# Kernel tuning notes

Measured on AMD Instinct MI355X. Metric: run time of the kernel, lower is better.

The kernel has to match this reference:

```python
import jax, jax.numpy as jnp
import numpy as np

NA, H, DIN, E, NN, ED = 1024, 128, 172, 256, 100000, 1
REG = 0.1
_gl_nodes = np.array([-0.1834346424956498, -0.525532409916329, -0.7966664774136267, -0.9602898564975363,
                      0.1834346424956498, 0.525532409916329, 0.7966664774136267, 0.9602898564975363], np.float32)
_gl_w = np.array([0.362683783378362, 0.3137066458778873, 0.2223810344533745, 0.1012285362903763] * 2, np.float32)
T_NODES = jnp.asarray(0.5 * (_gl_nodes + 1.0))    # tau = 1.0
T_WEIGHTS = jnp.asarray(0.5 * _gl_w)


def _rmsnorm(x, scale, eps=1e-8):
    rms = jnp.sqrt(jnp.sum(x * x, axis=-1, keepdims=True)) / np.sqrt(x.shape[-1])
    return scale * x / (rms + eps)


def setup_inputs() -> dict:
    key = jax.random.key(0)
    ks = jax.random.split(key, 16)
    s = 0.02
    return {
        "L_agg": 0.1 * jax.random.normal(ks[0], (NA, NA), jnp.float32),
        "delta_L_agg": 0.1 * jax.random.normal(ks[1], (NA, NA), jnp.float32),
        "x_sub": jax.random.normal(ks[2], (NA, DIN), jnp.float32),
        "m1_vec": jax.random.normal(ks[3], (NN, H), jnp.float32),
        "m2_vec": jax.random.normal(ks[4], (NN, H), jnp.float32),
        "names_table": jnp.zeros((NN, ED), jnp.float32),  # typ='Nil' static embedding
        "rms1_scale": jnp.ones((H,), jnp.float32),
        "rms2_scale": jnp.ones((H,), jnp.float32),
        "W_tune": s * jax.random.normal(ks[5], (DIN + 2 * ED, H), jnp.float32),
        "b_tune": jnp.zeros((H,), jnp.float32),
        "W_B1": s * jax.random.normal(ks[6], (H, H), jnp.float32),
        "b_B1": jnp.zeros((H,), jnp.float32),
        "W_B2": s * jax.random.normal(ks[7], (H, H), jnp.float32),
        "b_B2": jnp.zeros((H,), jnp.float32),
        "W_dt": 0.01 * jax.random.normal(ks[8], (H, 1), jnp.float32),
        "b_dt": -3.0 + 0.5 * jax.random.normal(ks[9], (1,), jnp.float32),  # softplus(b) small, like _init_dt_bias
        "A_log_1": jax.random.normal(ks[10], (H,), jnp.float32),
        "A_log_2": jax.random.normal(ks[11], (H,), jnp.float32),
        "target_src": jax.random.randint(ks[12], (E,), 0, NN),
        "target_dst": jax.random.randint(ks[13], (E,), 0, NN),
        "active_input_ids": jax.random.randint(ks[14], (NA,), 0, NN),
    }


def reference(L_agg, delta_L_agg, x_sub, m1_vec, m2_vec, names_table,
              rms1_scale, rms2_scale, W_tune, b_tune, W_B1, b_B1, W_B2, b_B2,
              W_dt, b_dt, A_log_1, A_log_2, target_src, target_dst, active_input_ids):
    n = L_agg.shape[0]
    I = jnp.eye(n, dtype=L_agg.dtype)
    # ZOH discretization of the graph Laplacian operator
    As_bar = I - REG * delta_L_agg + REG ** 2 * (delta_L_agg @ (L_agg + delta_L_agg / 2))
    dt = delta_L_agg[None] * T_NODES[:, None, None]                       # [8,n,n]
    LHS = I[None] - REG * dt + REG ** 2 * (dt @ (L_agg[None] + dt / 2))   # [8,n,n]
    P_L_inv = I - REG * L_agg
    # static-embedding neighbor info (zeros for 'Nil', done faithfully)
    neigh = jnp.zeros((n, 2 * ED), L_agg.dtype)
    neigh = neigh.at[:E, :ED].set(names_table[target_src])
    neigh = neigh.at[:E, ED:].set(names_table[target_dst])
    neigh = neigh.at[E:2 * E, :ED].set(names_table[target_dst])
    neigh = neigh.at[E:2 * E, ED:].set(names_table[target_src])
    x_in = jnp.concatenate([x_sub, neigh], axis=1)
    zt = x_in @ W_tune + b_tune                                           # TuneInput
    ztn = _rmsnorm(zt, rms1_scale)
    Bzt = ztn @ W_B1 + b_B1
    delta_1 = jax.nn.softplus(ztn @ W_dt + b_dt)                          # [n,1] broadcasts over H
    dA1 = delta_1 * (-jnp.exp(A_log_1))                                   # [n,H]
    At_bar_1 = jnp.exp(dA1)
    C_1 = (P_L_inv @ (Bzt * delta_1))[None] * T_WEIGHTS[:, None, None]    # [8,n,H]
    RHS_1 = jnp.exp(dA1[None] * T_NODES[:, None, None])                   # [8,n,H]
    integral_1 = jnp.sum((LHS @ C_1) * RHS_1, axis=0)                     # GL quadrature
    m1 = m1_vec[active_input_ids]
    updated_c_1 = As_bar @ (m1 * At_bar_1) + integral_1
    # second selective-SSM stage (reconstructed symmetrically from truncation)
    u_2 = zt + jax.nn.gelu(updated_c_1, approximate=True)
    u_2n = _rmsnorm(u_2, rms2_scale)
    But = u_2n @ W_B2 + b_B2
    delta_2 = jax.nn.softplus(u_2n @ W_dt + b_dt)
    dA2 = delta_2 * (-jnp.exp(A_log_2))
    At_bar_2 = jnp.exp(dA2)
    C_2 = (P_L_inv @ (But * delta_2))[None] * T_WEIGHTS[:, None, None]
    RHS_2 = jnp.exp(dA2[None] * T_NODES[:, None, None])
    integral_2 = jnp.sum((LHS @ C_2) * RHS_2, axis=0)
    m2 = m2_vec[active_input_ids]
    updated_c_2 = As_bar @ (m2 * At_bar_2) + integral_2
    return jnp.stack([updated_c_1, updated_c_2])                           # [2,n,H]
```

## Files before the change

kernel.cpp:

```cpp
#include <hip/hip_runtime.h>
#include <math.h>

#define N_A   1024
#define HDIM  128
#define DIN   172
#define E_CNT 256
#define LP    72

typedef __attribute__((ext_vector_type(8))) short bf16x8;
typedef __attribute__((ext_vector_type(4))) float f32x4;

__device__ __forceinline__ unsigned short f2bf(float x) {
    unsigned int u = __float_as_uint(x);
    unsigned int r = (u + 0x7fffu + ((u >> 16) & 1u)) >> 16;
    return (unsigned short)r;
}
__device__ __forceinline__ float bf2f(unsigned short x) {
    return __uint_as_float((unsigned int)x << 16);
}

__constant__ float c_t[8] = {
    0.4082826787521751f, 0.2372337950418355f, 0.10166676129318665f, 0.019855071751231843f,
    0.5917173212478249f, 0.7627662049581645f, 0.8983332387068134f, 0.9801449282487682f};
__constant__ float c_w[8] = {
    0.181341891689181f, 0.15685332293894365f, 0.11119051722668725f, 0.05061426814518815f,
    0.181341891689181f, 0.15685332293894365f, 0.11119051722668725f, 0.05061426814518815f};

__global__ __launch_bounds__(256)
void conv_all(const float* __restrict__ L, const float* __restrict__ dL,
              const float* __restrict__ x_sub, const float* __restrict__ names,
              const int* __restrict__ src, const int* __restrict__ dst,
              const float* __restrict__ W_tune, const float* __restrict__ W_B1,
              const float* __restrict__ W_B2,
              unsigned short* __restrict__ Lb, unsigned short* __restrict__ dLb,
              unsigned short* __restrict__ LbT, unsigned short* __restrict__ dLbT,
              unsigned short* __restrict__ Xb, unsigned short* __restrict__ WtT,
              unsigned short* __restrict__ WB1T, unsigned short* __restrict__ WB2T)
{
    __shared__ unsigned short tl[64][72];
    const int b = blockIdx.x, tid = threadIdx.x;
    if (b < 2048) {
        const int t = b * 256 + tid;
        const float* s = (t < 262144) ? L : dL;
        unsigned short* d = (t < 262144) ? Lb : dLb;
        const int q = (t < 262144) ? t : t - 262144;
        float4 v = *(const float4*)(s + (size_t)q * 4);
        ushort4 o;
        o.x = f2bf(v.x); o.y = f2bf(v.y); o.z = f2bf(v.z); o.w = f2bf(v.w);
        *(ushort4*)(d + (size_t)q * 4) = o;
    } else if (b < 2816) {
        const int t = (b - 2048) * 256 + tid;
        const int i = t / 192, k = t - i * 192;
        float val = 0.f;
        if (k < DIN) val = x_sub[(size_t)i * DIN + k];
        else if (k == DIN) {
            if (i < E_CNT)          val = names[src[i]];
            else if (i < 2 * E_CNT) val = names[dst[i - E_CNT]];
        } else if (k == DIN + 1) {
            if (i < E_CNT)          val = names[dst[i]];
            else if (i < 2 * E_CNT) val = names[src[i - E_CNT]];
        }
        Xb[t] = f2bf(val);
    } else if (b < 2912) {
        const int t = (b - 2816) * 256 + tid;
        const int j = t / 192, k = t - j * 192;
        WtT[t] = (k < DIN + 2) ? f2bf(W_tune[k * HDIM + j]) : (unsigned short)0;
    } else if (b < 3040) {
        const int t = (b - 2912) * 256 + tid;
        const int half = t >> 14, tt = t & 16383;
        const int j = tt >> 7, k = tt & 127;
        (half ? WB2T : WB1T)[tt] = f2bf((half ? W_B2 : W_B1)[k * HDIM + j]);
    } else {
        const int t = b - 3040;
        const float* s = (t < 256) ? L : dL;
        unsigned short* d = (t < 256) ? LbT : dLbT;
        const int tile = t & 255, tr = tile >> 4, tc = tile & 15;
        const int row = tid >> 2, cg = (tid & 3) << 4;
        #pragma unroll
        for (int e = 0; e < 4; ++e) {
            float4 v = *(const float4*)(s + (size_t)(tr * 64 + row) * 1024 + tc * 64 + cg + e * 4);
            tl[row][cg + e * 4 + 0] = f2bf(v.x);
            tl[row][cg + e * 4 + 1] = f2bf(v.y);
            tl[row][cg + e * 4 + 2] = f2bf(v.z);
            tl[row][cg + e * 4 + 3] = f2bf(v.w);
        }
        __syncthreads();
        unsigned short* drow = d + (size_t)(tc * 64 + row) * 1024 + tr * 64 + cg;
        #pragma unroll
        for (int e = 0; e < 4; ++e) {
            ushort4 o;
            o.x = tl[cg + e * 4 + 0][row];
            o.y = tl[cg + e * 4 + 1][row];
            o.z = tl[cg + e * 4 + 2][row];
            o.w = tl[cg + e * 4 + 3][row];
            *(ushort4*)(drow + e * 4) = o;
        }
    }
}

__device__ __forceinline__ void core_sa(
    const unsigned short* __restrict__ ag, const unsigned short* __restrict__ bg,
    unsigned short* As, unsigned short* Bs, int klen,
    int srow, int skc, int wrow, int wcol, int fr, int fk, f32x4 (&acc)[2][2])
{
    bf16x8 pa0 = *(const bf16x8*)ag, pa1 = *(const bf16x8*)(ag + 8);
    bf16x8 pb0 = *(const bf16x8*)bg, pb1 = *(const bf16x8*)(bg + 8);
    for (int k0 = 0; k0 < klen; k0 += 64) {
        __syncthreads();
        *(bf16x8*)&As[srow * LP + skc] = pa0; *(bf16x8*)&As[srow * LP + skc + 8] = pa1;
        *(bf16x8*)&Bs[srow * LP + skc] = pb0; *(bf16x8*)&Bs[srow * LP + skc + 8] = pb1;
        __syncthreads();
        if (k0 + 64 < klen) {
            pa0 = *(const bf16x8*)(ag + k0 + 64); pa1 = *(const bf16x8*)(ag + k0 + 72);
            pb0 = *(const bf16x8*)(bg + k0 + 64); pb1 = *(const bf16x8*)(bg + k0 + 72);
        }
        #pragma unroll
        for (int h = 0; h < 2; ++h) {
            const int ko = h * 32 + fk;
            bf16x8 a0 = *(const bf16x8*)&As[(wrow + fr) * LP + ko];
            bf16x8 a1 = *(const bf16x8*)&As[(wrow + 16 + fr) * LP + ko];
            bf16x8 b0 = *(const bf16x8*)&Bs[(wcol + fr) * LP + ko];
            bf16x8 b1 = *(const bf16x8*)&Bs[(wcol + 16 + fr) * LP + ko];
            acc[0][0] = __builtin_amdgcn_mfma_f32_16x16x32_bf16(a0, b0, acc[0][0], 0, 0, 0);
            acc[0][1] = __builtin_amdgcn_mfma_f32_16x16x32_bf16(a0, b1, acc[0][1], 0, 0, 0);
            acc[1][0] = __builtin_amdgcn_mfma_f32_16x16x32_bf16(a1, b0, acc[1][0], 0, 0, 0);
            acc[1][1] = __builtin_amdgcn_mfma_f32_16x16x32_bf16(a1, b1, acc[1][1], 0, 0, 0);
        }
    }
}

__global__ __launch_bounds__(256)
void k_d2(const unsigned short* __restrict__ LbT, const unsigned short* __restrict__ dLbT,
          const unsigned short* __restrict__ dLb,
          unsigned short* __restrict__ P1b, unsigned short* __restrict__ P2b,
          const unsigned short* __restrict__ Xb, const unsigned short* __restrict__ WtT,
          const float* __restrict__ b_tune, float* __restrict__ zt)
{
    __shared__ unsigned short shm[128 * LP];
    unsigned short* As = shm; unsigned short* Bs = shm + 64 * LP;
    const int bid = blockIdx.x, tid = threadIdx.x;
    const int srow = tid >> 2, skc = (tid & 3) << 4;
    const int lane = tid & 63, w = tid >> 6;
    const int wrow = (w >> 1) * 32, wcol = (w & 1) * 32;
    const int fr = lane & 15, fg = lane >> 4, fk = fg << 3;

    if (bid < 512) {
        const int bx = bid >> 4, rb = bid & 15;
        const int unit = bx >> 4, cb = bx & 15;
        const unsigned short* A = unit ? dLbT : LbT;
        unsigned short* O = unit ? P2b : P1b;
        const unsigned short* ag = A   + (size_t)(rb * 64 + srow) * 1024 + skc;
        const unsigned short* bg = dLb + (size_t)(cb * 64 + srow) * 1024 + skc;
        f32x4 acc[2][2] = {};
        core_sa(ag, bg, As, Bs, 1024, srow, skc, wrow, wcol, fr, fk, acc);
        #pragma unroll
        for (int m = 0; m < 2; ++m) {
            const int gm = rb * 64 + wrow + m * 16 + fg * 4;
            #pragma unroll
            for (int n = 0; n < 2; ++n) {
                const int gj = cb * 64 + wcol + n * 16 + fr;
                ushort4 tv;
                tv.x = f2bf(acc[m][n][0]); tv.y = f2bf(acc[m][n][1]);
                tv.z = f2bf(acc[m][n][2]); tv.w = f2bf(acc[m][n][3]);
                *(ushort4*)&O[(size_t)gj * 1024 + gm] = tv;
            }
        }
    } else {
        const int t = bid - 512;
        const int cb = t >> 4, rb = t & 15;
        const unsigned short* ag = Xb  + (size_t)(rb * 64 + srow) * 192 + skc;
        const unsigned short* bg = WtT + (size_t)(cb * 64 + srow) * 192 + skc;
        f32x4 acc[2][2] = {};
        core_sa(ag, bg, As, Bs, 192, srow, skc, wrow, wcol, fr, fk, acc);
        #pragma unroll
        for (int m = 0; m < 2; ++m) {
            const int gm = rb * 64 + wrow + m * 16 + fg * 4;
            #pragma unroll
            for (int n = 0; n < 2; ++n) {
                const int gj = cb * 64 + wcol + n * 16 + fr;
                const float bb = b_tune[gj];
                #pragma unroll
                for (int r = 0; r < 4; ++r)
                    zt[(size_t)(gm + r) * HDIM + gj] = acc[m][n][r] + bb;
            }
        }
    }
}

__device__ __forceinline__ float rowsum128(float v, float* red, int j)
{
    #pragma unroll
    for (int o = 32; o > 0; o >>= 1) v += __shfl_xor(v, o, 64);
    if ((j & 63) == 0) red[j >> 6] = v;
    __syncthreads();
    const float t = red[0] + red[1];
    __syncthreads();
    return t;
}

__device__ __forceinline__ void rms_core(
    float x, int i, int j,
    const float* rms_scale, const float* W_dt, const float* b_dt,
    const float* A_log, const float* m_vec, const int* act,
    unsigned short* xnb, float* VU, unsigned short* VUt, float* dlt, float* red)
{
    const float ss = rowsum128(x * x, red, j);
    const float rms = sqrtf(ss) * 0.08838834764831845f;
    const float xn = rms_scale[j] * x / (rms + 1e-8f);
    const float dsum = rowsum128(xn * W_dt[j], red, j);
    const float dd = dsum + b_dt[0];
    const float delta = dd > 0.f ? dd + log1pf(expf(-dd)) : log1pf(expf(dd));
    xnb[(size_t)i * HDIM + j] = f2bf(xn);
    const float U = m_vec[(size_t)act[i] * HDIM + j] * expf(-delta * expf(A_log[j]));
    VU[(size_t)i * 256 + 128 + j] = U;
    VUt[(size_t)(128 + j) * 1024 + i] = f2bf(U);
    if (j == 0) dlt[i] = delta;
}

__device__ __forceinline__ float post_elem(float y1, float y2, float y3, float s,
                                           float g, float u, float dA)
{
    const float bl = -0.1f * y1 + 0.01f * y2;
    const float cq = 0.005f * y3;
    float integ = 0.f;
    #pragma unroll
    for (int k = 0; k < 8; ++k) {
        const float t = c_t[k];
        integ += c_w[k] * (g + t * bl + t * t * cq) * expf(dA * t);
    }
    return u - 0.1f * s + integ;
}

__global__ __launch_bounds__(256)
void k_d3(const unsigned short* __restrict__ LbT,
          const unsigned short* __restrict__ P1b, const unsigned short* __restrict__ P2b,
          unsigned short* __restrict__ M2b, unsigned short* __restrict__ M3b,
          const float* __restrict__ zt,
          const float* __restrict__ rms1, const float* __restrict__ W_dt,
          const float* __restrict__ b_dt, const float* __restrict__ A1,
          const float* __restrict__ m1, const int* __restrict__ act,
          unsigned short* __restrict__ xnb, float* __restrict__ VU,
          unsigned short* __restrict__ VUt, float* __restrict__ dlt1)
{
    __shared__ unsigned short shm[128 * LP];
    const int bid = blockIdx.x, tid = threadIdx.x;

    if (bid < 512) {
        unsigned short* As = shm; unsigned short* Bs = shm + 64 * LP;
        const int srow = tid >> 2, skc = (tid & 3) << 4;
        const int lane = tid & 63, w = tid >> 6;
        const int wrow = (w >> 1) * 32, wcol = (w & 1) * 32;
        const int fr = lane & 15, fg = lane >> 4, fk = fg << 3;
        const int bx = bid >> 4, rb = bid & 15;
        const int unit = bx >> 4, cb = bx & 15;
        const unsigned short* Bt = unit ? P2b : P1b;
        const unsigned short* Src = unit ? P2b : P1b;
        unsigned short* O = unit ? M3b : M2b;
        const unsigned short* ag = LbT + (size_t)(rb * 64 + srow) * 1024 + skc;
        const unsigned short* bg = Bt  + (size_t)(cb * 64 + srow) * 1024 + skc;
        f32x4 acc[2][2] = {};
        core_sa(ag, bg, As, Bs, 1024, srow, skc, wrow, wcol, fr, fk, acc);
        #pragma unroll
        for (int m = 0; m < 2; ++m) {
            const int gm = rb * 64 + wrow + m * 16 + fg * 4;
            #pragma unroll
            for (int n = 0; n < 2; ++n) {
                const int gj = cb * 64 + wcol + n * 16 + fr;
                ushort4 sv = *(const ushort4*)&Src[(size_t)gj * 1024 + gm];
                ushort4 tv;
                tv.x = f2bf(bf2f(sv.x) - 0.1f * acc[m][n][0]);
                tv.y = f2bf(bf2f(sv.y) - 0.1f * acc[m][n][1]);
                tv.z = f2bf(bf2f(sv.z) - 0.1f * acc[m][n][2]);
                tv.w = f2bf(bf2f(sv.w) - 0.1f * acc[m][n][3]);
                *(ushort4*)&O[(size_t)gj * 1024 + gm] = tv;
            }
        }
    } else {
        float* redf = (float*)shm;
        const int g = tid >> 7, j = tid & 127;
        const int i = (bid - 512) * 2 + g;
        rms_core(zt[(size_t)i * HDIM + j], i, j, rms1, W_dt, b_dt, A1, m1, act,
                 xnb, VU, VUt, dlt1, redf + 2 * g);
    }
}

__global__ __launch_bounds__(256)
void gemm_bz2(const unsigned short* __restrict__ xnb, const unsigned short* __restrict__ WBT,
              const float* __restrict__ b_B, const float* __restrict__ dlt,
              float* __restrict__ VU, unsigned short* __restrict__ VUt)
{
    const int cb = blockIdx.x, rb = blockIdx.y;
    __shared__ unsigned short As[64 * LP];
    __shared__ unsigned short Bs[64 * LP];
    const int tid = threadIdx.x, srow = tid >> 2, skc = (tid & 3) << 4;
    const unsigned short* ag = xnb + (size_t)(rb * 64 + srow) * HDIM + skc;
    const unsigned short* bg = WBT + (size_t)(cb * 64 + srow) * HDIM + skc;
    const int lane = tid & 63, w = tid >> 6;
    const int wrow = (w >> 1) * 32, wcol = (w & 1) * 32;
    const int fr = lane & 15, fg = lane >> 4, fk = fg << 3;

    f32x4 acc[2][2] = {};
    core_sa(ag, bg, As, Bs, 128, srow, skc, wrow, wcol, fr, fk, acc);

    #pragma unroll
    for (int m = 0; m < 2; ++m) {
        const int gm = rb * 64 + wrow + m * 16 + fg * 4;
        #pragma unroll
        for (int n = 0; n < 2; ++n) {
            const int col = cb * 64 + wcol + n * 16 + fr;
            const float bb = b_B[col];
            float vv[4];
            #pragma unroll
            for (int r = 0; r < 4; ++r) {
                vv[r] = (acc[m][n][r] + bb) * dlt[gm + r];
                VU[(size_t)(gm + r) * 256 + col] = vv[r];
            }
            ushort4 tv;
            tv.x = f2bf(vv[0]); tv.y = f2bf(vv[1]); tv.z = f2bf(vv[2]); tv.w = f2bf(vv[3]);
            *(ushort4*)&VUt[(size_t)col * 1024 + gm] = tv;
        }
    }
}

__global__ __launch_bounds__(256)
void k_big(const unsigned short* __restrict__ Lb, const unsigned short* __restrict__ dLb,
           const unsigned short* __restrict__ P1b, const unsigned short* __restrict__ P2b,
           const unsigned short* __restrict__ M2b, const unsigned short* __restrict__ M3b,
           const unsigned short* __restrict__ VUt, const float* __restrict__ VU,
           float* __restrict__ Gf, float* __restrict__ dLVf, float* __restrict__ P1Vf,
           float* __restrict__ Y2f, float* __restrict__ Y3f, float* __restrict__ dLUf,
           float* __restrict__ P1Uf, float* __restrict__ P2Uf)
{
    __shared__ unsigned short shm[96 * LP];
    unsigned short* AsL = shm;
    unsigned short* Bs  = shm + 32 * LP;

    const int bid = blockIdx.x, tid = threadIdx.x;
    const int unit = bid >> 6, rem = bid & 63;
    const int rb = rem >> 1, cb = rem & 1;

    const unsigned short* A;
    float* O;
    switch (unit) {
        case 0: A = Lb;  O = Gf;   break;
        case 1: A = dLb; O = dLVf; break;
        case 2: A = P1b; O = P1Vf; break;
        case 3: A = M2b; O = Y2f;  break;
        case 4: A = M3b; O = Y3f;  break;
        case 5: A = dLb; O = dLUf; break;
        case 6: A = P1b; O = P1Uf; break;
        default: A = P2b; O = P2Uf; break;
    }
    const int bn0 = ((unit >= 5) ? 128 : 0) + cb * 64;

    const int sar = tid >> 3, sac = (tid & 7) << 3;
    const int sbr = tid >> 2, sbc = (tid & 3) << 4;

    const unsigned short* ag = A   + (size_t)(rb * 32 + sar) * 1024 + sac;
    const unsigned short* bg = VUt + (size_t)(bn0 + sbr) * 1024 + sbc;

    const int lane = tid & 63, w = tid >> 6;
    const int fr = lane & 15, fg = lane >> 4, fk = fg << 3;

    f32x4 acc[2] = {};
    bf16x8 pa = *(const bf16x8*)ag;
    bf16x8 pb0 = *(const bf16x8*)bg, pb1 = *(const bf16x8*)(bg + 8);

    for (int k0 = 0; k0 < 1024; k0 += 64) {
        __syncthreads();
        *(bf16x8*)&AsL[sar * LP + sac] = pa;
        *(bf16x8*)&Bs[sbr * LP + sbc] = pb0; *(bf16x8*)&Bs[sbr * LP + sbc + 8] = pb1;
        __syncthreads();
        if (k0 + 64 < 1024) {
            pa = *(const bf16x8*)(ag + k0 + 64);
            pb0 = *(const bf16x8*)(bg + k0 + 64); pb1 = *(const bf16x8*)(bg + k0 + 72);
        }
        #pragma unroll
        for (int h = 0; h < 2; ++h) {
            const int ko = h * 32 + fk;
            bf16x8 a0 = *(const bf16x8*)&AsL[fr * LP + ko];
            bf16x8 a1 = *(const bf16x8*)&AsL[(16 + fr) * LP + ko];
            bf16x8 b0 = *(const bf16x8*)&Bs[(w * 16 + fr) * LP + ko];
            acc[0] = __builtin_amdgcn_mfma_f32_16x16x32_bf16(a0, b0, acc[0], 0, 0, 0);
            acc[1] = __builtin_amdgcn_mfma_f32_16x16x32_bf16(a1, b0, acc[1], 0, 0, 0);
        }
    }

    #pragma unroll
    for (int m = 0; m < 2; ++m) {
        const int gm = rb * 32 + m * 16 + fg * 4;
        const int gj = cb * 64 + w * 16 + fr;
        if (unit == 0) {
            #pragma unroll
            for (int r = 0; r < 4; ++r)
                O[(size_t)(gm + r) * 128 + gj] =
                    VU[(size_t)(gm + r) * 256 + gj] - 0.1f * acc[m][r];
        } else {
            #pragma unroll
            for (int r = 0; r < 4; ++r)
                O[(size_t)(gm + r) * 128 + gj] = acc[m][r];
        }
    }
}

__global__ __launch_bounds__(256)
void k_mid(const float* __restrict__ Gf, const float* __restrict__ dLVf,
           const float* __restrict__ P1Vf, const float* __restrict__ Y2f,
           const float* __restrict__ Y3f, const float* __restrict__ dLUf,
           const float* __restrict__ P1Uf, const float* __restrict__ P2Uf,
           const float* __restrict__ zt, const float* __restrict__ dlt1,
           const float* __restrict__ A1,
           const float* __restrict__ rms2, const float* __restrict__ W_dt,
           const float* __restrict__ b_dt, const float* __restrict__ A2,
           const float* __restrict__ m2, const int* __restrict__ act,
           unsigned short* __restrict__ xnb, float* __restrict__ VU,
           unsigned short* __restrict__ VUt, float* __restrict__ dlt2,
           float* __restrict__ out0)
{
    __shared__ float redf[4];
    const int tid = threadIdx.x;
    const int g = tid >> 7, j = tid & 127;
    const int i = blockIdx.x * 2 + g;
    const int idx = i * HDIM + j;

    const float y1 = dLVf[idx] - 0.1f * P1Vf[idx];
    const float s  = dLUf[idx] - 0.1f * P1Uf[idx] - 0.05f * P2Uf[idx];
    const float dA = -dlt1[i] * expf(A1[j]);
    const float o1 = post_elem(y1, Y2f[idx], Y3f[idx], s, Gf[idx],
                               VU[(size_t)i * 256 + 128 + j], dA);
    out0[idx] = o1;
    const float g3 = o1 * o1 * o1;
    const float gel = 0.5f * o1 * (1.0f + tanhf(0.7978845608028654f * (o1 + 0.044715f * g3)));
    const float x = zt[idx] + gel;

    rms_core(x, i, j, rms2, W_dt, b_dt, A2, m2, act, xnb, VU, VUt, dlt2, redf + 2 * g);
}

__global__ __launch_bounds__(256)
void k_tail(const float* __restrict__ Gf, const float* __restrict__ dLVf,
            const float* __restrict__ P1Vf, const float* __restrict__ Y2f,
            const float* __restrict__ Y3f, const float* __restrict__ dLUf,
            const float* __restrict__ P1Uf, const float* __restrict__ P2Uf,
            const float* __restrict__ VU, const float* __restrict__ dlt,
            const float* __restrict__ A_log, float* __restrict__ out)
{
    const int idx = blockIdx.x * 256 + threadIdx.x;
    const int i = idx >> 7, j = idx & 127;
    const float y1 = dLVf[idx] - 0.1f * P1Vf[idx];
    const float s  = dLUf[idx] - 0.1f * P1Uf[idx] - 0.05f * P2Uf[idx];
    const float dA = -dlt[i] * expf(A_log[j]);
    out[idx] = post_elem(y1, Y2f[idx], Y3f[idx], s, Gf[idx],
                         VU[(size_t)i * 256 + 128 + j], dA);
}

extern "C" void kernel_launch(void* const* d_in, const int* in_sizes, int n_in,
                              void* d_out, int out_size, void* d_ws, size_t ws_size,
                              hipStream_t stream)
{
    const float* L      = (const float*)d_in[0];
    const float* dL     = (const float*)d_in[1];
    const float* x_sub  = (const float*)d_in[2];
    const float* m1     = (const float*)d_in[3];
    const float* m2     = (const float*)d_in[4];
    const float* names  = (const float*)d_in[5];
    const float* rms1   = (const float*)d_in[6];
    const float* rms2   = (const float*)d_in[7];
    const float* W_tune = (const float*)d_in[8];
    const float* b_tune = (const float*)d_in[9];
    const float* W_B1   = (const float*)d_in[10];
    const float* b_B1   = (const float*)d_in[11];
    const float* W_B2   = (const float*)d_in[12];
    const float* b_B2   = (const float*)d_in[13];
    const float* W_dt   = (const float*)d_in[14];
    const float* b_dt   = (const float*)d_in[15];
    const float* A1     = (const float*)d_in[16];
    const float* A2     = (const float*)d_in[17];
    const int*   src    = (const int*)d_in[18];
    const int*   dst    = (const int*)d_in[19];
    const int*   act    = (const int*)d_in[20];
    float* out = (float*)d_out;

    float* ws    = (float*)d_ws;
    float* zt    = ws;
    float* VU    = zt    + 131072;
    float* Gf    = VU    + 262144;
    float* dLVf  = Gf    + 131072;
    float* P1Vf  = dLVf  + 131072;
    float* Y2f   = P1Vf  + 131072;
    float* Y3f   = Y2f   + 131072;
    float* dLUf  = Y3f   + 131072;
    float* P1Uf  = dLUf  + 131072;
    float* P2Uf  = P1Uf  + 131072;
    float* dlt1  = P2Uf  + 131072;
    float* dlt2  = dlt1  + 1024;
    unsigned short* Lb    = (unsigned short*)(dlt2 + 1024);
    unsigned short* dLb   = Lb    + 1048576;
    unsigned short* LbT   = dLb   + 1048576;
    unsigned short* dLbT  = LbT   + 1048576;
    unsigned short* M2b   = dLbT;
    unsigned short* P1b   = dLbT  + 1048576;
    unsigned short* P2b   = P1b   + 1048576;
    unsigned short* M3b   = P2b   + 1048576;
    unsigned short* VUt   = M3b   + 1048576;
    unsigned short* Xb    = VUt   + 262144;
    unsigned short* WtT   = Xb    + 196608;
    unsigned short* WB1T  = WtT   + 24576;
    unsigned short* WB2T  = WB1T  + 16384;
    unsigned short* xnb   = WB2T  + 16384;

    conv_all<<<dim3(3552), dim3(256), 0, stream>>>(
        L, dL, x_sub, names, src, dst, W_tune, W_B1, W_B2,
        Lb, dLb, LbT, dLbT, Xb, WtT, WB1T, WB2T);

    k_d2<<<dim3(544), dim3(256), 0, stream>>>(
        LbT, dLbT, dLb, P1b, P2b, Xb, WtT, b_tune, zt);

    k_d3<<<dim3(1024), dim3(256), 0, stream>>>(
        LbT, P1b, P2b, M2b, M3b, zt,
        rms1, W_dt, b_dt, A1, m1, act, xnb, VU, VUt, dlt1);

    gemm_bz2<<<dim3(2, 16), dim3(256), 0, stream>>>(xnb, WB1T, b_B1, dlt1, VU, VUt);

    k_big<<<dim3(512), dim3(256), 0, stream>>>(
        Lb, dLb, P1b, P2b, M2b, M3b, VUt, VU,
        Gf, dLVf, P1Vf, Y2f, Y3f, dLUf, P1Uf, P2Uf);

    k_mid<<<dim3(512), dim3(256), 0, stream>>>(
        Gf, dLVf, P1Vf, Y2f, Y3f, dLUf, P1Uf, P2Uf,
        zt, dlt1, A1, rms2, W_dt, b_dt, A2, m2, act,
        xnb, VU, VUt, dlt2, out);

    gemm_bz2<<<dim3(2, 16), dim3(256), 0, stream>>>(xnb, WB2T, b_B2, dlt2, VU, VUt);

    k_big<<<dim3(512), dim3(256), 0, stream>>>(
        Lb, dLb, P1b, P2b, M2b, M3b, VUt, VU,
        Gf, dLVf, P1Vf, Y2f, Y3f, dLUf, P1Uf, P2Uf);

    k_tail<<<dim3(512), dim3(256), 0, stream>>>(
        Gf, dLVf, P1Vf, Y2f, Y3f, dLUf, P1Uf, P2Uf,
        VU, dlt2, A2, out + 131072);
}
```

Baseline: 77.46 us.

## Fuse RMSNorm/delta stage with B-projection GEMM, removing separate gemm_bz2 launches

Folds the RMSNorm, softplus delta and U computation together with the small xn@W_B GEMM into one task per 16-row by 64-column tile. Each block keeps the normalized rows in LDS and runs MFMA on them directly, so the xnb round trip and two kernel launches go away. The cost is that the row-wise norm is recomputed once for each of the two column blocks. The second-stage U moves to a separate U2 buffer so the fused kernel does not overwrite VU values still being read by other blocks.

```diff
diff --git a/kernel.cpp b/kernel.cpp
--- a/kernel.cpp
+++ b/kernel.cpp
@@ -198,25 +198,6 @@
     return t;
 }
 
-__device__ __forceinline__ void rms_core(
-    float x, int i, int j,
-    const float* rms_scale, const float* W_dt, const float* b_dt,
-    const float* A_log, const float* m_vec, const int* act,
-    unsigned short* xnb, float* VU, unsigned short* VUt, float* dlt, float* red)
-{
-    const float ss = rowsum128(x * x, red, j);
-    const float rms = sqrtf(ss) * 0.08838834764831845f;
-    const float xn = rms_scale[j] * x / (rms + 1e-8f);
-    const float dsum = rowsum128(xn * W_dt[j], red, j);
-    const float dd = dsum + b_dt[0];
-    const float delta = dd > 0.f ? dd + log1pf(expf(-dd)) : log1pf(expf(dd));
-    xnb[(size_t)i * HDIM + j] = f2bf(xn);
-    const float U = m_vec[(size_t)act[i] * HDIM + j] * expf(-delta * expf(A_log[j]));
-    VU[(size_t)i * 256 + 128 + j] = U;
-    VUt[(size_t)(128 + j) * 1024 + i] = f2bf(U);
-    if (j == 0) dlt[i] = delta;
-}
-
 __device__ __forceinline__ float post_elem(float y1, float y2, float y3, float s,
                                            float g, float u, float dA)
 {
@@ -229,6 +210,80 @@
         integ += c_w[k] * (g + t * bl + t * t * cq) * expf(dA * t);
     }
     return u - 0.1f * s + integ;
+}
+
+__device__ void rmsbz_task(int cb, int rb, int tid,
+    unsigned short* xnL , float* dltL , float* red ,
+    const float* zt,
+    const float* Gf, const float* dLVf, const float* P1Vf, const float* Y2f,
+    const float* Y3f, const float* dLUf, const float* P1Uf, const float* P2Uf,
+    const float* dlt_prev, const float* A_prev, float* out0,
+    const float* rms_scale, const float* W_dt, const float* b_dt,
+    const float* A_log, const float* m_vec, const int* act,
+    const unsigned short* WBT, const float* b_B,
+    float* VU, unsigned short* VUt, float* Udst, int ustride,
+    float* dlt_out)
+{
+    const int g = tid >> 7, j = tid & 127;
+
+    for (int rr = 0; rr < 8; ++rr) {
+        const int lr = g * 8 + rr;
+        const int row = rb * 16 + lr;
+        const int idx = row * HDIM + j;
+        float x;
+        if (!out0) {
+            x = zt[idx];
+        } else {
+            const float y1 = dLVf[idx] - 0.1f * P1Vf[idx];
+            const float s  = dLUf[idx] - 0.1f * P1Uf[idx] - 0.05f * P2Uf[idx];
+            const float dA = -dlt_prev[row] * expf(A_prev[j]);
+            const float o1 = post_elem(y1, Y2f[idx], Y3f[idx], s, Gf[idx],
+                                       VU[(size_t)row * 256 + 128 + j], dA);
+            if (cb == 0) out0[idx] = o1;
+            const float g3 = o1 * o1 * o1;
+            const float gel = 0.5f * o1 * (1.0f + tanhf(0.7978845608028654f * (o1 + 0.044715f * g3)));
+            x = zt[idx] + gel;
+        }
+        const float ss = rowsum128(x * x, red + 2 * g, j);
+        const float rms = sqrtf(ss) * 0.08838834764831845f;
+        const float xn = rms_scale[j] * x / (rms + 1e-8f);
+        const float ds = rowsum128(xn * W_dt[j], red + 2 * g, j);
+        const float dd = ds + b_dt[0];
+        const float delta = dd > 0.f ? dd + log1pf(expf(-dd)) : log1pf(expf(dd));
+        xnL[lr * 136 + j] = f2bf(xn);
+        if (j == 0) dltL[lr] = delta;
+        if (cb == 0) {
+            const float U = m_vec[(size_t)act[row] * HDIM + j] * expf(-delta * expf(A_log[j]));
+            Udst[(size_t)row * ustride + j] = U;
+            VUt[(size_t)(128 + j) * 1024 + row] = f2bf(U);
+            if (j == 0) dlt_out[row] = delta;
+        }
+    }
+    __syncthreads();
+
+    const int lane = tid & 63, w = tid >> 6;
+    const int fr = lane & 15, fg = lane >> 4, fk = fg << 3;
+    const int col = cb * 64 + w * 16 + fr;
+
+    f32x4 acc = {};
+    #pragma unroll
+    for (int ks = 0; ks < 4; ++ks) {
+        const int ko = ks * 32 + fk;
+        bf16x8 a = *(const bf16x8*)&xnL[fr * 136 + ko];
+        bf16x8 b = *(const bf16x8*)(WBT + (size_t)col * HDIM + ko);
+        acc = __builtin_amdgcn_mfma_f32_16x16x32_bf16(a, b, acc, 0, 0, 0);
+    }
+    const float bb = b_B[col];
+    const int r0 = fg * 4;
+    float vv[4];
+    #pragma unroll
+    for (int r = 0; r < 4; ++r) {
+        vv[r] = (acc[r] + bb) * dltL[r0 + r];
+        VU[(size_t)(rb * 16 + r0 + r) * 256 + col] = vv[r];
+    }
+    ushort4 tv;
+    tv.x = f2bf(vv[0]); tv.y = f2bf(vv[1]); tv.z = f2bf(vv[2]); tv.w = f2bf(vv[3]);
+    *(ushort4*)&VUt[(size_t)col * 1024 + rb * 16 + r0] = tv;
 }
 
 __global__ __launch_bounds__(256)
@@ -239,8 +294,9 @@
           const float* __restrict__ rms1, const float* __restrict__ W_dt,
           const float* __restrict__ b_dt, const float* __restrict__ A1,
           const float* __restrict__ m1, const int* __restrict__ act,
-          unsigned short* __restrict__ xnb, float* __restrict__ VU,
-          unsigned short* __restrict__ VUt, float* __restrict__ dlt1)
+          const unsigned short* __restrict__ WB1T, const float* __restrict__ b_B1,
+          float* __restrict__ VU, unsigned short* __restrict__ VUt,
+          float* __restrict__ dlt1)
 {
     __shared__ unsigned short shm[128 * LP];
     const int bid = blockIdx.x, tid = threadIdx.x;
@@ -254,7 +310,6 @@
         const int bx = bid >> 4, rb = bid & 15;
         const int unit = bx >> 4, cb = bx & 15;
         const unsigned short* Bt = unit ? P2b : P1b;
-        const unsigned short* Src = unit ? P2b : P1b;
         unsigned short* O = unit ? M3b : M2b;
         const unsigned short* ag = LbT + (size_t)(rb * 64 + srow) * 1024 + skc;
         const unsigned short* bg = Bt  + (size_t)(cb * 64 + srow) * 1024 + skc;
@@ -266,7 +321,7 @@
             #pragma unroll
             for (int n = 0; n < 2; ++n) {
                 const int gj = cb * 64 + wcol + n * 16 + fr;
-                ushort4 sv = *(const ushort4*)&Src[(size_t)gj * 1024 + gm];
+                ushort4 sv = *(const ushort4*)&Bt[(size_t)gj * 1024 + gm];
                 ushort4 tv;
                 tv.x = f2bf(bf2f(sv.x) - 0.1f * acc[m][n][0]);
                 tv.y = f2bf(bf2f(sv.y) - 0.1f * acc[m][n][1]);
@@ -276,49 +331,16 @@
             }
         }
     } else {
-        float* redf = (float*)shm;
-        const int g = tid >> 7, j = tid & 127;
-        const int i = (bid - 512) * 2 + g;
-        rms_core(zt[(size_t)i * HDIM + j], i, j, rms1, W_dt, b_dt, A1, m1, act,
-                 xnb, VU, VUt, dlt1, redf + 2 * g);
-    }
-}
-
-__global__ __launch_bounds__(256)
-void gemm_bz2(const unsigned short* __restrict__ xnb, const unsigned short* __restrict__ WBT,
-              const float* __restrict__ b_B, const float* __restrict__ dlt,
-              float* __restrict__ VU, unsigned short* __restrict__ VUt)
-{
-    const int cb = blockIdx.x, rb = blockIdx.y;
-    __shared__ unsigned short As[64 * LP];
-    __shared__ unsigned short Bs[64 * LP];
-    const int tid = threadIdx.x, srow = tid >> 2, skc = (tid & 3) << 4;
-    const unsigned short* ag = xnb + (size_t)(rb * 64 + srow) * HDIM + skc;
-    const unsigned short* bg = WBT + (size_t)(cb * 64 + srow) * HDIM + skc;
-    const int lane = tid & 63, w = tid >> 6;
-    const int wrow = (w >> 1) * 32, wcol = (w & 1) * 32;
-    const int fr = lane & 15, fg = lane >> 4, fk = fg << 3;
-
-    f32x4 acc[2][2] = {};
-    core_sa(ag, bg, As, Bs, 128, srow, skc, wrow, wcol, fr, fk, acc);
-
-    #pragma unroll
-    for (int m = 0; m < 2; ++m) {
-        const int gm = rb * 64 + wrow + m * 16 + fg * 4;
-        #pragma unroll
-        for (int n = 0; n < 2; ++n) {
-            const int col = cb * 64 + wcol + n * 16 + fr;
-            const float bb = b_B[col];
-            float vv[4];
-            #pragma unroll
-            for (int r = 0; r < 4; ++r) {
-                vv[r] = (acc[m][n][r] + bb) * dlt[gm + r];
-                VU[(size_t)(gm + r) * 256 + col] = vv[r];
-            }
-            ushort4 tv;
-            tv.x = f2bf(vv[0]); tv.y = f2bf(vv[1]); tv.z = f2bf(vv[2]); tv.w = f2bf(vv[3]);
-            *(ushort4*)&VUt[(size_t)col * 1024 + gm] = tv;
-        }
+        unsigned short* xnL = shm;
+        float* dltL = (float*)(shm + 16 * 136);
+        float* red  = dltL + 16;
+        const int t = bid - 512;
+        const int cb = t >> 6, rb = t & 63;
+        rmsbz_task(cb, rb, tid, xnL, dltL, red, zt,
+                   nullptr, nullptr, nullptr, nullptr, nullptr, nullptr, nullptr, nullptr,
+                   nullptr, nullptr, nullptr,
+                   rms1, W_dt, b_dt, A1, m1, act, WB1T, b_B1,
+                   VU, VUt, VU + 128, 256, dlt1);
     }
 }
 
@@ -413,27 +435,21 @@
            const float* __restrict__ rms2, const float* __restrict__ W_dt,
            const float* __restrict__ b_dt, const float* __restrict__ A2,
            const float* __restrict__ m2, const int* __restrict__ act,
-           unsigned short* __restrict__ xnb, float* __restrict__ VU,
-           unsigned short* __restrict__ VUt, float* __restrict__ dlt2,
+           const unsigned short* __restrict__ WB2T, const float* __restrict__ b_B2,
+           float* __restrict__ VU, unsigned short* __restrict__ VUt,
+           float* __restrict__ U2, float* __restrict__ dlt2,
            float* __restrict__ out0)
 {
-    __shared__ float redf[4];
-    const int tid = threadIdx.x;
-    const int g = tid >> 7, j = tid & 127;
-    const int i = blockIdx.x * 2 + g;
-    const int idx = i * HDIM + j;
-
-    const float y1 = dLVf[idx] - 0.1f * P1Vf[idx];
-    const float s  = dLUf[idx] - 0.1f * P1Uf[idx] - 0.05f * P2Uf[idx];
-    const float dA = -dlt1[i] * expf(A1[j]);
-    const float o1 = post_elem(y1, Y2f[idx], Y3f[idx], s, Gf[idx],
-                               VU[(size_t)i * 256 + 128 + j], dA);
-    out0[idx] = o1;
-    const float g3 = o1 * o1 * o1;
-    const float gel = 0.5f * o1 * (1.0f + tanhf(0.7978845608028654f * (o1 + 0.044715f * g3)));
-    const float x = zt[idx] + gel;
-
-    rms_core(x, i, j, rms2, W_dt, b_dt, A2, m2, act, xnb, VU, VUt, dlt2, redf + 2 * g);
+    __shared__ unsigned short shm[16 * 136 + 48];
+    unsigned short* xnL = shm;
+    float* dltL = (float*)(shm + 16 * 136);
+    float* red  = dltL + 16;
+    const int cb = blockIdx.x >> 6, rb = blockIdx.x & 63;
+    rmsbz_task(cb, rb, threadIdx.x, xnL, dltL, red, zt,
+               Gf, dLVf, P1Vf, Y2f, Y3f, dLUf, P1Uf, P2Uf,
+               dlt1, A1, out0,
+               rms2, W_dt, b_dt, A2, m2, act, WB2T, b_B2,
+               VU, VUt, U2, 128, dlt2);
 }
 
 __global__ __launch_bounds__(256)
@@ -441,7 +457,7 @@
             const float* __restrict__ P1Vf, const float* __restrict__ Y2f,
             const float* __restrict__ Y3f, const float* __restrict__ dLUf,
             const float* __restrict__ P1Uf, const float* __restrict__ P2Uf,
-            const float* __restrict__ VU, const float* __restrict__ dlt,
+            const float* __restrict__ U2, const float* __restrict__ dlt,
             const float* __restrict__ A_log, float* __restrict__ out)
 {
     const int idx = blockIdx.x * 256 + threadIdx.x;
@@ -449,8 +465,7 @@
     const float y1 = dLVf[idx] - 0.1f * P1Vf[idx];
     const float s  = dLUf[idx] - 0.1f * P1Uf[idx] - 0.05f * P2Uf[idx];
     const float dA = -dlt[i] * expf(A_log[j]);
-    out[idx] = post_elem(y1, Y2f[idx], Y3f[idx], s, Gf[idx],
-                         VU[(size_t)i * 256 + 128 + j], dA);
+    out[idx] = post_elem(y1, Y2f[idx], Y3f[idx], s, Gf[idx], U2[idx], dA);
 }
 
 extern "C" void kernel_launch(void* const* d_in, const int* in_sizes, int n_in,
@@ -483,7 +498,8 @@
     float* ws    = (float*)d_ws;
     float* zt    = ws;
     float* VU    = zt    + 131072;
-    float* Gf    = VU    + 262144;
+    float* U2    = VU    + 262144;
+    float* Gf    = U2    + 131072;
     float* dLVf  = Gf    + 131072;
     float* P1Vf  = dLVf  + 131072;
     float* Y2f   = P1Vf  + 131072;
@@ -506,7 +522,6 @@
     unsigned short* WtT   = Xb    + 196608;
     unsigned short* WB1T  = WtT   + 24576;
     unsigned short* WB2T  = WB1T  + 16384;
-    unsigned short* xnb   = WB2T  + 16384;
 
     conv_all<<<dim3(3552), dim3(256), 0, stream>>>(
         L, dL, x_sub, names, src, dst, W_tune, W_B1, W_B2,
@@ -515,22 +530,19 @@
     k_d2<<<dim3(544), dim3(256), 0, stream>>>(
         LbT, dLbT, dLb, P1b, P2b, Xb, WtT, b_tune, zt);
 
-    k_d3<<<dim3(1024), dim3(256), 0, stream>>>(
+    k_d3<<<dim3(640), dim3(256), 0, stream>>>(
         LbT, P1b, P2b, M2b, M3b, zt,
-        rms1, W_dt, b_dt, A1, m1, act, xnb, VU, VUt, dlt1);
-
-    gemm_bz2<<<dim3(2, 16), dim3(256), 0, stream>>>(xnb, WB1T, b_B1, dlt1, VU, VUt);
+        rms1, W_dt, b_dt, A1, m1, act, WB1T, b_B1,
+        VU, VUt, dlt1);
 
     k_big<<<dim3(512), dim3(256), 0, stream>>>(
         Lb, dLb, P1b, P2b, M2b, M3b, VUt, VU,
         Gf, dLVf, P1Vf, Y2f, Y3f, dLUf, P1Uf, P2Uf);
 
-    k_mid<<<dim3(512), dim3(256), 0, stream>>>(
+    k_mid<<<dim3(128), dim3(256), 0, stream>>>(
         Gf, dLVf, P1Vf, Y2f, Y3f, dLUf, P1Uf, P2Uf,
         zt, dlt1, A1, rms2, W_dt, b_dt, A2, m2, act,
-        xnb, VU, VUt, dlt2, out);
-
-    gemm_bz2<<<dim3(2, 16), dim3(256), 0, stream>>>(xnb, WB2T, b_B2, dlt2, VU, VUt);
+        WB2T, b_B2, VU, VUt, U2, dlt2, out);
 
     k_big<<<dim3(512), dim3(256), 0, stream>>>(
         Lb, dLb, P1b, P2b, M2b, M3b, VUt, VU,
@@ -538,5 +550,5 @@
 
     k_tail<<<dim3(512), dim3(256), 0, stream>>>(
         Gf, dLVf, P1Vf, Y2f, Y3f, dLUf, P1Uf, P2Uf,
-        VU, dlt2, A2, out + 131072);
-}
+        U2, dlt2, A2, out + 131072);
+}
```

New measurement: 91.21 us, median of 2. +17.8%, slower.
